# Optimization experiments

Hardware: AMD Instinct MI355X
Metric: run time of the kernel (lower is better)

The kernel has to match this reference:

```python
import jax, jax.numpy as jnp
import numpy as np

D_IN = 1024      # points per target cloud
SPACE = 3        # spatial dim
BOTT = 64        # bottleneck size
GP = 4           # grid points per axis -> G = GP**SPACE = 64
BATCH = 2


def _linear_params(key, fan_in, fan_out):
    # torch.nn.Linear default init: U(-1/sqrt(fan_in), 1/sqrt(fan_in))
    lim = 1.0 / np.sqrt(fan_in)
    kw, kb = jax.random.split(key)
    W = jax.random.uniform(kw, (fan_in, fan_out), minval=-lim, maxval=lim, dtype=jnp.float32)
    b = jax.random.uniform(kb, (fan_out,), minval=-lim, maxval=lim, dtype=jnp.float32)
    return W, b


def setup_inputs() -> dict:
    key = jax.random.key(0)
    ks = jax.random.split(key, 8)
    x = jax.random.normal(ks[0], (BATCH, D_IN, SPACE), dtype=jnp.float32)
    # grid of GP**SPACE points in [0,1]^SPACE (np.meshgrid as in the module)
    axes = [np.linspace(0.0, 1.0, GP, dtype=np.float32) for _ in range(SPACE)]
    grid = jnp.asarray(np.stack(np.meshgrid(*axes), axis=-1).reshape(-1, SPACE))  # [G, 3]
    We1, be1 = _linear_params(ks[1], D_IN * SPACE, 512)
    We2, be2 = _linear_params(ks[2], 512, 128)
    We3, be3 = _linear_params(ks[3], 128, BOTT)
    Wd1, bd1 = _linear_params(ks[4], BOTT + SPACE, 128)
    Wd2, bd2 = _linear_params(ks[5], 128, 512)
    Wd3, bd3 = _linear_params(ks[6], 512, D_IN * SPACE)
    return {"x": x, "grid": grid,
            "We1": We1, "be1": be1, "We2": We2, "be2": be2, "We3": We3, "be3": be3,
            "Wd1": Wd1, "bd1": bd1, "Wd2": Wd2, "bd2": bd2, "Wd3": Wd3, "bd3": bd3}


def reference(x, grid, We1, be1, We2, be2, We3, be3, Wd1, bd1, Wd2, bd2, Wd3, bd3):
    B = x.shape[0]
    G = grid.shape[0]
    # encoder: flatten cloud -> latent  [B, BOTT]
    xf = x.reshape(B, -1)
    h = jax.nn.relu(xf @ We1 + be1)
    h = jax.nn.relu(h @ We2 + be2)
    z = jax.nn.relu(h @ We3 + be3)
    # decoder: concat(latent, grid point) for every grid point  [B, G, BOTT+SPACE]
    zi = jnp.concatenate([
        jnp.broadcast_to(z[:, None, :], (B, G, z.shape[-1])),
        jnp.broadcast_to(grid[None, :, :], (B, G, SPACE)),
    ], axis=-1)
    d = jax.nn.relu(zi @ Wd1 + bd1)
    d = jax.nn.relu(d @ Wd2 + bd2)
    d = jnp.tanh(d @ Wd3 + bd3)            # [B, G, D_IN*SPACE]
    Y = d.reshape(B, G * D_IN, SPACE)      # generated point set, N = G*D_IN
    S = x                                  # target point set,   M = D_IN
    # pairwise squared distances [B, N, M] via ||y||^2 + ||s||^2 - 2 y.s
    d2 = ((Y * Y).sum(-1)[:, :, None]
          + (S * S).sum(-1)[:, None, :]
          - 2.0 * jnp.einsum('bnd,bmd->bnm', Y, S))
    # symmetric chamfer: sum of min over each direction
    loss = jnp.sum(jnp.min(d2, axis=2)) + jnp.sum(jnp.min(d2, axis=1))
    return loss
```

## Files before the change

kernel.cpp:

```cpp
#include <hip/hip_runtime.h>

#define NB 2
#define NPTS 1024
#define NGEN 65536

#define OFF_GW    0
#define OFF_H1P   8192
#define OFF_D2H   32768
#define OFF_S4    98304
#define OFF_Y4    106496
#define OFF_WT4   630784
#define OFF_MPART 2203648

__global__ __launch_bounds__(256) void kA_init(
    const float* __restrict__ x, const float* __restrict__ grid,
    const float* __restrict__ Wd1, const float* __restrict__ Wd3,
    const float* __restrict__ We1,
    float* __restrict__ gw, float* __restrict__ S4,
    float4* __restrict__ Wt4, float* __restrict__ h1part) {
  if (blockIdx.x < 64) {
    int t = blockIdx.x * 256 + threadIdx.x;
    if (t < 8192) {
      int g = t >> 7, j = t & 127;
      float a = grid[g * 3 + 0] * Wd1[64 * 128 + j]
              + grid[g * 3 + 1] * Wd1[65 * 128 + j]
              + grid[g * 3 + 2] * Wd1[66 * 128 + j];
      gw[t] = a;
    } else if (t < 10240) {
      int p = t - 8192;
      const float* xp = x + p * 3;
      float s0 = xp[0], s1 = xp[1], s2 = xp[2];
      ((float4*)S4)[p] = make_float4(s0, s1, s2, s0 * s0 + s1 * s1 + s2 * s2);
    }
  } else if (blockIdx.x < 1600) {
    int tid = (blockIdx.x - 64) * 256 + threadIdx.x;
    int p  = tid & 1023;
    int k4 = (tid >> 10) & 127;
    int c  = tid >> 17;
    const float* W = Wd3 + (k4 * 4) * 3072 + p * 3 + c;
    float w0 = W[0], w1 = W[3072], w2 = W[2 * 3072], w3 = W[3 * 3072];
    Wt4[(c * 128 + k4) * 1024 + p] = make_float4(w0, w1, w2, w3);
  } else {
    int idx = blockIdx.x - 1600;
    int kc = idx % 24;
    int rest = idx / 24;
    int jh = rest & 1;
    int b  = rest >> 1;
    int j = jh * 256 + threadIdx.x;
    const float* xb = x + b * 3072 + kc * 128;
    const float* W  = We1 + (kc * 128) * 512 + j;
    float acc = 0.f;
#pragma unroll 8
    for (int k = 0; k < 128; ++k) acc += xb[k] * W[k * 512];
    h1part[kc * 1024 + b * 512 + j] = acc;
  }
}

__global__ __launch_bounds__(256) void kB_enc_dec2(
    const float* __restrict__ h1part, const float* __restrict__ be1,
    const float* __restrict__ We2, const float* __restrict__ be2,
    const float* __restrict__ We3, const float* __restrict__ be3,
    const float* __restrict__ Wd1, const float* __restrict__ bd1,
    const float* __restrict__ gw,
    const float* __restrict__ Wd2, const float* __restrict__ bd2,
    float* __restrict__ d2h) {
  __shared__ float h1l[512];
  __shared__ float h2p[2][128];
  __shared__ float h2l[128];
  __shared__ float zl[64];
  __shared__ float d1[128];
  int bg = blockIdx.x;
  int b = bg >> 6, g = bg & 63;
  int t = threadIdx.x;
#pragma unroll
  for (int i = 0; i < 2; ++i) {
    int k = i * 256 + t;
    float a = be1[k];
#pragma unroll
    for (int kc = 0; kc < 24; ++kc) a += h1part[kc * 1024 + b * 512 + k];
    h1l[k] = fmaxf(a, 0.f);
  }
  __syncthreads();
  {
    int j = t & 127, half = t >> 7;
    const float* W = We2 + (half * 256) * 128 + j;
    const float* h = h1l + half * 256;
    float a = 0.f;
#pragma unroll 8
    for (int k = 0; k < 256; ++k) a += h[k] * W[k * 128];
    h2p[half][j] = a;
  }
  __syncthreads();
  if (t < 128) h2l[t] = fmaxf(h2p[0][t] + h2p[1][t] + be2[t], 0.f);
  __syncthreads();
  if (t < 64) {
    float a = be3[t];
#pragma unroll 4
    for (int k = 0; k < 128; ++k) a += h2l[k] * We3[k * 64 + t];
    zl[t] = fmaxf(a, 0.f);
  }
  __syncthreads();
  if (t < 128) {
    float a = bd1[t];
#pragma unroll 4
    for (int k = 0; k < 64; ++k) a += zl[k] * Wd1[k * 128 + t];
    d1[t] = fmaxf(a + gw[g * 128 + t], 0.f);
  }
  __syncthreads();
  float a0 = bd2[t], a1 = bd2[t + 256];
#pragma unroll 4
  for (int k = 0; k < 128; ++k) {
    float dv = d1[k];
    a0 += dv * Wd2[k * 512 + t];
    a1 += dv * Wd2[k * 512 + t + 256];
  }
  float* o = d2h + bg * 512;
  o[t] = fmaxf(a0, 0.f);
  o[t + 256] = fmaxf(a1, 0.f);
}

__global__ __launch_bounds__(512) void kC_dec3_y4(
    const float* __restrict__ d2h, const float4* __restrict__ Wt4,
    const float* __restrict__ bd3, float4* __restrict__ Y4,
    float* __restrict__ out) {
  __shared__ float4 a_lds[8 * 128];
  __shared__ float part[8 * 3 * 8 * 64];
  int rt = blockIdx.x >> 4;
  int pg = blockIdx.x & 15;
  int t = threadIdx.x;
  if (blockIdx.x == 0 && t == 0) out[0] = 0.f;
  {
    const float4* src = (const float4*)d2h + rt * 1024;
#pragma unroll
    for (int i = 0; i < 2; ++i) a_lds[i * 512 + t] = src[i * 512 + t];
  }
  __syncthreads();
  int lane = t & 63, w = t >> 6;
  int p = pg * 64 + lane;
  const float4* wp0 = Wt4 + p;
  const float4* wp1 = Wt4 + 131072 + p;
  const float4* wp2 = Wt4 + 262144 + p;
  float acc[8][3];
#pragma unroll
  for (int r = 0; r < 8; ++r)
#pragma unroll
    for (int c = 0; c < 3; ++c) acc[r][c] = 0.f;
  int kbase = w * 16;
#pragma unroll 4
  for (int i = 0; i < 16; ++i) {
    int k4 = kbase + i;
    float4 w0 = wp0[k4 * 1024];
    float4 w1 = wp1[k4 * 1024];
    float4 w2 = wp2[k4 * 1024];
#pragma unroll
    for (int r = 0; r < 8; ++r) {
      float4 A = a_lds[r * 128 + k4];
      acc[r][0] += A.x * w0.x + A.y * w0.y + A.z * w0.z + A.w * w0.w;
      acc[r][1] += A.x * w1.x + A.y * w1.y + A.z * w1.z + A.w * w1.w;
      acc[r][2] += A.x * w2.x + A.y * w2.y + A.z * w2.z + A.w * w2.w;
    }
  }
#pragma unroll
  for (int r = 0; r < 8; ++r)
#pragma unroll
    for (int c = 0; c < 3; ++c)
      part[((r * 3 + c) * 8 + w) * 64 + lane] = acc[r][c];
  __syncthreads();
  {
    int r = w;
    float s0 = 0.f, s1 = 0.f, s2 = 0.f;
#pragma unroll
    for (int ww = 0; ww < 8; ++ww) {
      s0 += part[((r * 3 + 0) * 8 + ww) * 64 + lane];
      s1 += part[((r * 3 + 1) * 8 + ww) * 64 + lane];
      s2 += part[((r * 3 + 2) * 8 + ww) * 64 + lane];
    }
    float b0 = bd3[p * 3], b1 = bd3[p * 3 + 1], b2 = bd3[p * 3 + 2];
    float y0 = tanhf(s0 + b0), y1 = tanhf(s1 + b1), y2 = tanhf(s2 + b2);
    int row = rt * 8 + r;
    Y4[row * 1024 + p] = make_float4(-2.f * y0, -2.f * y1, -2.f * y2,
                                     y0 * y0 + y1 * y1 + y2 * y2);
  }
}

__global__ __launch_bounds__(256) void kD_chamfer(
    const float4* __restrict__ Y4, const float4* __restrict__ S4,
    float* __restrict__ mpart, float* __restrict__ out) {
  __shared__ float4 c_lds[1024];
  int t = threadIdx.x;
  if (blockIdx.x < 256) {
    int b = blockIdx.x >> 7, nt = blockIdx.x & 127;
    {
      const float4* src = S4 + b * 1024;
#pragma unroll
      for (int i = 0; i < 4; ++i) c_lds[i * 256 + t] = src[i * 256 + t];
    }
    float4 my0 = Y4[b * 65536 + nt * 512 + t];
    float4 my1 = Y4[b * 65536 + nt * 512 + 256 + t];
    __syncthreads();
    float mn0 = __builtin_inff(), mn1 = mn0;
#pragma unroll 8
    for (int m = 0; m < 1024; ++m) {
      float4 s = c_lds[m];
      float d0 = __builtin_fmaf(s.x, my0.x,
                 __builtin_fmaf(s.y, my0.y,
                 __builtin_fmaf(s.z, my0.z, s.w)));
      float d1 = __builtin_fmaf(s.x, my1.x,
                 __builtin_fmaf(s.y, my1.y,
                 __builtin_fmaf(s.z, my1.z, s.w)));
      mn0 = fminf(mn0, d0);
      mn1 = fminf(mn1, d1);
    }
    float v = (mn0 + my0.w) + (mn1 + my1.w);
#pragma unroll
    for (int off = 32; off > 0; off >>= 1) v += __shfl_down(v, off);
    __shared__ float bsum[4];
    int lane = t & 63, w = t >> 6;
    if (lane == 0) bsum[w] = v;
    __syncthreads();
    if (t == 0) atomicAdd(out, bsum[0] + bsum[1] + bsum[2] + bsum[3]);
  } else {
    int blk = blockIdx.x - 256;
    int b   = blk >> 7;
    int mg  = (blk >> 6) & 1;
    int nch = blk & 63;
    {
      const float4* src = Y4 + b * 65536 + nch * 1024;
#pragma unroll
      for (int i = 0; i < 4; ++i) c_lds[i * 256 + t] = src[i * 256 + t];
    }
    float4 s0 = S4[b * 1024 + mg * 512 + t];
    float4 s1 = S4[b * 1024 + mg * 512 + 256 + t];
    __syncthreads();
    float mn0 = __builtin_inff(), mn1 = mn0;
#pragma unroll 8
    for (int n = 0; n < 1024; ++n) {
      float4 y = c_lds[n];
      float d0 = __builtin_fmaf(y.x, s0.x,
                 __builtin_fmaf(y.y, s0.y,
                 __builtin_fmaf(y.z, s0.z, y.w)));
      float d1 = __builtin_fmaf(y.x, s1.x,
                 __builtin_fmaf(y.y, s1.y,
                 __builtin_fmaf(y.z, s1.z, y.w)));
      mn0 = fminf(mn0, d0);
      mn1 = fminf(mn1, d1);
    }
    int base = (nch * 2 + b) * 1024 + mg * 512;
    mpart[base + t]       = mn0 + s0.w;
    mpart[base + 256 + t] = mn1 + s1.w;
  }
}

__global__ __launch_bounds__(256) void kE_dir2_reduce(
    const float* __restrict__ mpart, float* __restrict__ out) {
  int gid = blockIdx.x * 256 + threadIdx.x;
  int b = gid >> 10, m = gid & 1023;
  float v = __builtin_inff();
#pragma unroll 8
  for (int ch = 0; ch < 64; ++ch)
    v = fminf(v, mpart[(ch * 2 + b) * 1024 + m]);
#pragma unroll
  for (int off = 32; off > 0; off >>= 1) v += __shfl_down(v, off);
  __shared__ float bsum[4];
  int lane = threadIdx.x & 63, w = threadIdx.x >> 6;
  if (lane == 0) bsum[w] = v;
  __syncthreads();
  if (threadIdx.x == 0) atomicAdd(out, bsum[0] + bsum[1] + bsum[2] + bsum[3]);
}

extern "C" void kernel_launch(void* const* d_in, const int* in_sizes, int n_in,
                              void* d_out, int out_size, void* d_ws, size_t ws_size,
                              hipStream_t stream) {
  const float* x   = (const float*)d_in[0];
  const float* grd = (const float*)d_in[1];
  const float* We1 = (const float*)d_in[2];
  const float* be1 = (const float*)d_in[3];
  const float* We2 = (const float*)d_in[4];
  const float* be2 = (const float*)d_in[5];
  const float* We3 = (const float*)d_in[6];
  const float* be3 = (const float*)d_in[7];
  const float* Wd1 = (const float*)d_in[8];
  const float* bd1 = (const float*)d_in[9];
  const float* Wd2 = (const float*)d_in[10];
  const float* bd2 = (const float*)d_in[11];
  const float* Wd3 = (const float*)d_in[12];
  const float* bd3 = (const float*)d_in[13];
  float* ws = (float*)d_ws;
  float* out = (float*)d_out;

  float* gw     = ws + OFF_GW;
  float* h1part = ws + OFF_H1P;
  float* d2h    = ws + OFF_D2H;
  float* S4     = ws + OFF_S4;
  float* Y4     = ws + OFF_Y4;
  float4* Wt4   = (float4*)(ws + OFF_WT4);
  float* mpart  = ws + OFF_MPART;

  hipLaunchKernelGGL(kA_init, dim3(1696), dim3(256), 0, stream,
                     x, grd, Wd1, Wd3, We1, gw, S4, Wt4, h1part);
  hipLaunchKernelGGL(kB_enc_dec2, dim3(128), dim3(256), 0, stream,
                     h1part, be1, We2, be2, We3, be3, Wd1, bd1, gw, Wd2, bd2,
                     d2h);
  hipLaunchKernelGGL(kC_dec3_y4, dim3(256), dim3(512), 0, stream,
                     d2h, Wt4, bd3, (float4*)Y4, out);
  hipLaunchKernelGGL(kD_chamfer, dim3(512), dim3(256), 0, stream,
                     (const float4*)Y4, (const float4*)S4, mpart, out);
  hipLaunchKernelGGL(kE_dir2_reduce, dim3(8), dim3(256), 0, stream,
                     mpart, out);
}
```

Baseline: 186.0 us.

## Split encoder into per-batch kernel and fuse dec2 into dec3 kernel

The encoder chain is now computed once per batch in a 2-block kernel that writes z@Wd1+bd1 (zw), rather than redundantly in 128 blocks (one per batch/grid point). The Wd2 layer moves into the dec3 kernel: each block rebuilds its 8 d1 rows from zw+gw, computes d2 directly into LDS, and no longer round-trips d2h through global memory. The trade-off is that each of the 256 dec3 blocks recomputes an 8x128x512 matmul, reading all of Wd2, and the 2-block encoder leaves most of the GPU idle during its serial phase.

```diff
diff --git a/kernel.cpp b/kernel.cpp
--- a/kernel.cpp
+++ b/kernel.cpp
@@ -6,11 +6,11 @@
 
 #define OFF_GW    0
 #define OFF_H1P   8192
-#define OFF_D2H   32768
-#define OFF_S4    98304
-#define OFF_Y4    106496
-#define OFF_WT4   630784
-#define OFF_MPART 2203648
+#define OFF_ZW    32768
+#define OFF_S4    33280
+#define OFF_Y4    41472
+#define OFF_WT4   565760
+#define OFF_MPART 2138624
 
 __global__ __launch_bounds__(256) void kA_init(
     const float* __restrict__ x, const float* __restrict__ grid,
@@ -56,83 +56,110 @@
   }
 }
 
-__global__ __launch_bounds__(256) void kB_enc_dec2(
+__global__ __launch_bounds__(512) void kB_enc(
     const float* __restrict__ h1part, const float* __restrict__ be1,
     const float* __restrict__ We2, const float* __restrict__ be2,
     const float* __restrict__ We3, const float* __restrict__ be3,
     const float* __restrict__ Wd1, const float* __restrict__ bd1,
-    const float* __restrict__ gw,
-    const float* __restrict__ Wd2, const float* __restrict__ bd2,
-    float* __restrict__ d2h) {
+    float* __restrict__ zw, float* __restrict__ out) {
   __shared__ float h1l[512];
-  __shared__ float h2p[2][128];
+  __shared__ float h2p[512];
   __shared__ float h2l[128];
+  __shared__ float zp[512];
   __shared__ float zl[64];
-  __shared__ float d1[128];
-  int bg = blockIdx.x;
-  int b = bg >> 6, g = bg & 63;
+  __shared__ float wp[512];
+  int b = blockIdx.x;
   int t = threadIdx.x;
-#pragma unroll
-  for (int i = 0; i < 2; ++i) {
-    int k = i * 256 + t;
-    float a = be1[k];
-#pragma unroll
-    for (int kc = 0; kc < 24; ++kc) a += h1part[kc * 1024 + b * 512 + k];
-    h1l[k] = fmaxf(a, 0.f);
-  }
-  __syncthreads();
-  {
-    int j = t & 127, half = t >> 7;
-    const float* W = We2 + (half * 256) * 128 + j;
-    const float* h = h1l + half * 256;
+  if (b == 0 && t == 0) out[0] = 0.f;
+  {
+    float a = be1[t];
+#pragma unroll
+    for (int kc = 0; kc < 24; ++kc) a += h1part[kc * 1024 + b * 512 + t];
+    h1l[t] = fmaxf(a, 0.f);
+  }
+  __syncthreads();
+  {
+    int q = t >> 7, j = t & 127;
+    const float* W = We2 + (q * 128) * 128 + j;
+    const float* h = h1l + q * 128;
     float a = 0.f;
-#pragma unroll 8
-    for (int k = 0; k < 256; ++k) a += h[k] * W[k * 128];
-    h2p[half][j] = a;
-  }
-  __syncthreads();
-  if (t < 128) h2l[t] = fmaxf(h2p[0][t] + h2p[1][t] + be2[t], 0.f);
+#pragma unroll 16
+    for (int k = 0; k < 128; ++k) a += h[k] * W[k * 128];
+    h2p[t] = a;
+  }
+  __syncthreads();
+  if (t < 128)
+    h2l[t] = fmaxf(h2p[t] + h2p[128 + t] + h2p[256 + t] + h2p[384 + t]
+                   + be2[t], 0.f);
+  __syncthreads();
+  {
+    int q = t >> 6, j = t & 63;
+    float a = 0.f;
+#pragma unroll
+    for (int kk = 0; kk < 16; ++kk) {
+      int k = q * 16 + kk;
+      a += h2l[k] * We3[k * 64 + j];
+    }
+    zp[t] = a;
+  }
   __syncthreads();
   if (t < 64) {
     float a = be3[t];
-#pragma unroll 4
-    for (int k = 0; k < 128; ++k) a += h2l[k] * We3[k * 64 + t];
+#pragma unroll
+    for (int q = 0; q < 8; ++q) a += zp[q * 64 + t];
     zl[t] = fmaxf(a, 0.f);
   }
   __syncthreads();
-  if (t < 128) {
-    float a = bd1[t];
-#pragma unroll 4
-    for (int k = 0; k < 64; ++k) a += zl[k] * Wd1[k * 128 + t];
-    d1[t] = fmaxf(a + gw[g * 128 + t], 0.f);
-  }
-  __syncthreads();
-  float a0 = bd2[t], a1 = bd2[t + 256];
-#pragma unroll 4
-  for (int k = 0; k < 128; ++k) {
-    float dv = d1[k];
-    a0 += dv * Wd2[k * 512 + t];
-    a1 += dv * Wd2[k * 512 + t + 256];
-  }
-  float* o = d2h + bg * 512;
-  o[t] = fmaxf(a0, 0.f);
-  o[t + 256] = fmaxf(a1, 0.f);
-}
-
-__global__ __launch_bounds__(512) void kC_dec3_y4(
-    const float* __restrict__ d2h, const float4* __restrict__ Wt4,
-    const float* __restrict__ bd3, float4* __restrict__ Y4,
-    float* __restrict__ out) {
+  {
+    int q = t >> 7, j = t & 127;
+    float a = 0.f;
+#pragma unroll
+    for (int kk = 0; kk < 16; ++kk) {
+      int k = q * 16 + kk;
+      a += zl[k] * Wd1[k * 128 + j];
+    }
+    wp[t] = a;
+  }
+  __syncthreads();
+  if (t < 128)
+    zw[b * 128 + t] = wp[t] + wp[128 + t] + wp[256 + t] + wp[384 + t]
+                      + bd1[t];
+}
+
+__global__ __launch_bounds__(512) void kC_dec23_y4(
+    const float* __restrict__ zw, const float* __restrict__ gw,
+    const float* __restrict__ Wd2, const float* __restrict__ bd2,
+    const float4* __restrict__ Wt4, const float* __restrict__ bd3,
+    float4* __restrict__ Y4) {
   __shared__ float4 a_lds[8 * 128];
   __shared__ float part[8 * 3 * 8 * 64];
+  __shared__ float d1l[8 * 128];
   int rt = blockIdx.x >> 4;
   int pg = blockIdx.x & 15;
   int t = threadIdx.x;
-  if (blockIdx.x == 0 && t == 0) out[0] = 0.f;
-  {
-    const float4* src = (const float4*)d2h + rt * 1024;
-#pragma unroll
-    for (int i = 0; i < 2; ++i) a_lds[i * 512 + t] = src[i * 512 + t];
+#pragma unroll
+  for (int i = 0; i < 2; ++i) {
+    int idx = i * 512 + t;
+    int r = idx >> 7, kk = idx & 127;
+    int row = rt * 8 + r, b = row >> 6, g = row & 63;
+    d1l[idx] = fmaxf(zw[b * 128 + kk] + gw[g * 128 + kk], 0.f);
+  }
+  __syncthreads();
+  {
+    float* a_f = (float*)a_lds;
+    int j = t;
+    float bj = bd2[j];
+    float acc[8];
+#pragma unroll
+    for (int r = 0; r < 8; ++r) acc[r] = bj;
+#pragma unroll 8
+    for (int k = 0; k < 128; ++k) {
+      float wv = Wd2[k * 512 + j];
+#pragma unroll
+      for (int r = 0; r < 8; ++r) acc[r] += d1l[r * 128 + k] * wv;
+    }
+#pragma unroll
+    for (int r = 0; r < 8; ++r) a_f[r * 512 + j] = fmaxf(acc[r], 0.f);
   }
   __syncthreads();
   int lane = t & 63, w = t >> 6;
@@ -290,7 +317,7 @@
 
   float* gw     = ws + OFF_GW;
   float* h1part = ws + OFF_H1P;
-  float* d2h    = ws + OFF_D2H;
+  float* zw     = ws + OFF_ZW;
   float* S4     = ws + OFF_S4;
   float* Y4     = ws + OFF_Y4;
   float4* Wt4   = (float4*)(ws + OFF_WT4);
@@ -298,11 +325,10 @@
 
   hipLaunchKernelGGL(kA_init, dim3(1696), dim3(256), 0, stream,
                      x, grd, Wd1, Wd3, We1, gw, S4, Wt4, h1part);
-  hipLaunchKernelGGL(kB_enc_dec2, dim3(128), dim3(256), 0, stream,
-                     h1part, be1, We2, be2, We3, be3, Wd1, bd1, gw, Wd2, bd2,
-                     d2h);
-  hipLaunchKernelGGL(kC_dec3_y4, dim3(256), dim3(512), 0, stream,
-                     d2h, Wt4, bd3, (float4*)Y4, out);
+  hipLaunchKernelGGL(kB_enc, dim3(2), dim3(512), 0, stream,
+                     h1part, be1, We2, be2, We3, be3, Wd1, bd1, zw, out);
+  hipLaunchKernelGGL(kC_dec23_y4, dim3(256), dim3(512), 0, stream,
+                     zw, gw, Wd2, bd2, Wt4, bd3, (float4*)Y4);
   hipLaunchKernelGGL(kD_chamfer, dim3(512), dim3(256), 0, stream,
                      (const float4*)Y4, (const float4*)S4, mpart, out);
   hipLaunchKernelGGL(kE_dir2_reduce, dim3(8), dim3(256), 0, stream,
```

Measured after the change: 165.8 us. -10.9%, faster.
